# Kernel tuning notes

Hardware: AMD Instinct MI355X
Metric: run time of the kernel (lower is better)

## Reference

```python
import jax, jax.numpy as jnp
import numpy as np

N, D, H, C, E, ED, HID = 50000, 160, 5, 32, 800000, 16, 512
EPS = 1e-5  # torch LayerNorm default
NEG_SLOPE = 0.2  # GATv2Conv default negative_slope


def layer_norm(x, g, b):
    mu = x.mean(-1, keepdims=True)
    var = x.var(-1, keepdims=True)  # biased, matches torch LayerNorm
    return (x - mu) * jax.lax.rsqrt(var + EPS) * g + b


def setup_inputs() -> dict:
    key = jax.random.key(0)
    ks = jax.random.split(key, 12)
    p = lambda k, shape: jax.random.normal(k, shape, jnp.float32) * 0.05
    z = lambda *s: jnp.zeros(s, jnp.float32)
    o = lambda *s: jnp.ones(s, jnp.float32)
    return {
        "x": jax.random.normal(ks[0], (N, D), jnp.float32),
        "edge_index": jax.random.randint(ks[1], (2, E), 0, N),
        "edge_attr": jax.random.normal(ks[2], (E, ED), jnp.float32),
        "u": jax.random.normal(ks[3], (1024, 64), jnp.float32),
        "batch": jax.random.randint(ks[4], (N,), 0, 1024),
        # GATv2Conv params (lin_l, lin_r, lin_edge, att, bias)
        "Wl": p(ks[5], (D, H * C)), "bl": z(H * C),
        "Wr": p(ks[6], (D, H * C)), "br": z(H * C),
        "We": p(ks[7], (ED, H * C)),
        "att": p(ks[8], (H, C)),
        "b_gat": z(H * C),
        # norm1
        "g1": o(D), "b1": z(D),
        # output MLP: Linear(D,HID) -> SELU -> LayerNorm(HID) -> Linear(HID,D)
        "W_m1": p(ks[9], (D, HID)), "b_m1": z(HID),
        "g_m": o(HID), "b_m": z(HID),
        "W_m2": p(ks[10], (HID, D)), "b_m2": z(D),
        # norm2
        "g2": o(D), "b2": z(D),
    }


def reference(x, edge_index, edge_attr, u, batch, Wl, bl, Wr, br, We, att, b_gat,
              g1, b1, W_m1, b_m1, g_m, b_m, W_m2, b_m2, g2, b2):
    src, dst = edge_index[0], edge_index[1]  # messages flow src -> dst
    xl = (x @ Wl + bl).reshape(N, H, C)      # source projection
    xr = (x @ Wr + br).reshape(N, H, C)      # target projection
    ea = (edge_attr @ We).reshape(E, H, C)
    # GATv2 scoring: att . leaky_relu(x_l[j] + x_r[i] + e_ij)
    e = jax.nn.leaky_relu(xl[src] + xr[dst] + ea, NEG_SLOPE)   # [E,H,C]
    score = jnp.einsum('ehc,hc->eh', e, att)                   # [E,H]
    # segment softmax over incoming edges of each target node
    mx = jax.ops.segment_max(score, dst, num_segments=N)       # [N,H]
    ex = jnp.exp(score - mx[dst])
    denom = jax.ops.segment_sum(ex, dst, num_segments=N)
    alpha = ex / denom[dst]                                    # [E,H]
    agg = jax.ops.segment_sum(alpha[:, :, None] * xl[src], dst, num_segments=N)
    attn = agg.reshape(N, H * C) + b_gat                       # concat heads
    # residual + norm, MLP, residual + norm (dropout=0)
    out = layer_norm(x + attn, g1, b1)
    h = layer_norm(jax.nn.selu(out @ W_m1 + b_m1), g_m, b_m)
    mlp = h @ W_m2 + b_m2
    return layer_norm(out + mlp, g2, b2)
```

## Files before the change

### kernel.cpp

```cpp
#include <hip/hip_runtime.h>
#include <math.h>

#define N_NODES 50000
#define D 160
#define H 5
#define C 32
#define HC 160
#define E_EDGES 800000
#define ED 16
#define HID 512
#define EPS 1e-5f
#define NEG_SLOPE 0.2f

typedef __attribute__((ext_vector_type(8))) short bf16x8;
typedef __attribute__((ext_vector_type(4))) float f32x4;
typedef __attribute__((ext_vector_type(4))) short short4v;

__device__ inline float bf2f(short s) {
  unsigned u = ((unsigned)(unsigned short)s) << 16;
  return __builtin_bit_cast(float, u);
}
__device__ inline short f2bf(float f) {
  unsigned u = __builtin_bit_cast(unsigned, f);
  u = u + 0x7fffu + ((u >> 16) & 1u);
  return (short)(u >> 16);
}
__device__ inline float selu_f(float v) {
  return 1.0507009873554805f * (v > 0.f ? v : 1.6732632423543772f * (__expf(v) - 1.f));
}

__global__ void prep_weights(const float* __restrict__ Wl, const float* __restrict__ Wr,
                             const float* __restrict__ Wm1, const float* __restrict__ Wm2,
                             const float* __restrict__ We,
                             short* __restrict__ WlT, short* __restrict__ WrT,
                             short* __restrict__ W1T, short* __restrict__ W2T,
                             short* __restrict__ WeTp) {
  int i = blockIdx.x * blockDim.x + threadIdx.x;
  if (i < 25600) { int n = i / 160, k = i % 160; WlT[n*160 + k] = f2bf(Wl[k*160 + n]); return; }
  i -= 25600;
  if (i < 25600) { int n = i / 160, k = i % 160; WrT[n*160 + k] = f2bf(Wr[k*160 + n]); return; }
  i -= 25600;
  if (i < 81920) { int n = i / 160, k = i % 160; W1T[n*160 + k] = f2bf(Wm1[k*512 + n]); return; }
  i -= 81920;
  if (i < 81920) { int n = i / 512, k = i % 512; W2T[n*512 + k] = f2bf(Wm2[k*160 + n]); return; }
  i -= 81920;
  if (i < 5120) { int col = i / 32, k = i % 32;
    WeTp[col*32 + k] = (k < ED) ? f2bf(We[k*160 + col]) : (short)0; }
}

__global__ void convert_x(const float* __restrict__ x, short* __restrict__ xb) {
  int i = blockIdx.x * blockDim.x + threadIdx.x;
  if (i < N_NODES * D / 8) {
    const float4* s = (const float4*)(x + (size_t)i * 8);
    float4 a = s[0], b = s[1];
    bf16x8 o;
    o[0] = f2bf(a.x); o[1] = f2bf(a.y); o[2] = f2bf(a.z); o[3] = f2bf(a.w);
    o[4] = f2bf(b.x); o[5] = f2bf(b.y); o[6] = f2bf(b.z); o[7] = f2bf(b.w);
    *(bf16x8*)(xb + (size_t)i * 8) = o;
  }
}

__global__ __launch_bounds__(256) void proj_mfma(
    const short* __restrict__ xb, const short* __restrict__ WlT, const short* __restrict__ WrT,
    const float* __restrict__ bl, const float* __restrict__ br,
    short* __restrict__ xl, short* __restrict__ xr)
{
  __shared__ short As[64][40];
  int t = threadIdx.x;
  int wave = t >> 6, lane = t & 63;
  int lq = lane >> 4, lc = lane & 15;
  int row0 = blockIdx.x * 64;
  f32x4 accl[10] = {}, accr[10] = {};
  for (int kt = 0; kt < 5; ++kt) {
    int k0 = kt * 32;
    {
      int r = t >> 2, seg = t & 3;
      int gr = min(row0 + r, N_NODES - 1);
      bf16x8 v = *(const bf16x8*)&xb[(size_t)gr * 160 + k0 + seg * 8];
      *(bf16x8*)&As[r][seg * 8] = v;
    }
    __syncthreads();
    bf16x8 af = *(bf16x8*)&As[wave * 16 + lc][lq * 8];
#pragma unroll
    for (int ct = 0; ct < 10; ++ct) {
      int cc = ct * 16 + lc;
      bf16x8 bfl = *(const bf16x8*)&WlT[cc * 160 + k0 + lq * 8];
      accl[ct] = __builtin_amdgcn_mfma_f32_16x16x32_bf16(af, bfl, accl[ct], 0, 0, 0);
      bf16x8 bfr = *(const bf16x8*)&WrT[cc * 160 + k0 + lq * 8];
      accr[ct] = __builtin_amdgcn_mfma_f32_16x16x32_bf16(af, bfr, accr[ct], 0, 0, 0);
    }
    __syncthreads();
  }
#pragma unroll
  for (int ct = 0; ct < 10; ++ct) {
    int col = ct * 16 + lc;
    float bbl = bl[col], bbr = br[col];
#pragma unroll
    for (int rg = 0; rg < 4; ++rg) {
      int row = row0 + wave * 16 + lq * 4 + rg;
      if (row < N_NODES) {
        xl[(size_t)row * 160 + col] = f2bf(accl[ct][rg] + bbl);
        xr[(size_t)row * 160 + col] = f2bf(accr[ct][rg] + bbr);
      }
    }
  }
}

__global__ void count_kernel(const int* __restrict__ ei, int* __restrict__ cnt) {
  int e = blockIdx.x * blockDim.x + threadIdx.x;
  if (e < E_EDGES) atomicAdd(&cnt[ei[E_EDGES + e]], 1);
}

__global__ __launch_bounds__(1024) void scan_kernel(const int* __restrict__ cnt,
                                                    int* __restrict__ offs) {
  const int PER = (N_NODES + 1023) / 1024;
  int t = threadIdx.x;
  int start = t * PER;
  int sum = 0;
  for (int i = 0; i < PER; ++i) {
    int idx = start + i;
    if (idx < N_NODES) sum += cnt[idx];
  }
  int lane = t & 63, wid = t >> 6;
  int v = sum;
  for (int off = 1; off < 64; off <<= 1) {
    int u = __shfl_up(v, off, 64);
    if (lane >= off) v += u;
  }
  __shared__ int wsums[16];
  if (lane == 63) wsums[wid] = v;
  __syncthreads();
  if (wid == 0) {
    int w = (lane < 16) ? wsums[lane] : 0;
    for (int off = 1; off < 16; off <<= 1) {
      int u = __shfl_up(w, off, 64);
      if (lane >= off) w += u;
    }
    if (lane < 16) wsums[lane] = w;
  }
  __syncthreads();
  int excl = v - sum + (wid > 0 ? wsums[wid - 1] : 0);
  int run = excl;
  for (int i = 0; i < PER; ++i) {
    int idx = start + i;
    if (idx < N_NODES) { offs[idx] = run; run += cnt[idx]; }
  }
  if (t == 1023) offs[N_NODES] = run;
}

__global__ void scatter3(const int* __restrict__ ei, const float* __restrict__ eattr,
                         const int* __restrict__ offs, int* __restrict__ cursor,
                         int* __restrict__ srcm, int* __restrict__ dstm,
                         short* __restrict__ eacsr) {
  int e = blockIdx.x * blockDim.x + threadIdx.x;
  if (e < E_EDGES) {
    int dst = ei[E_EDGES + e];
    int src = ei[e];
    int slot = atomicAdd(&cursor[dst], 1);
    int j = offs[dst] + slot;
    srcm[j] = src * 160;
    dstm[j] = dst * 160;
    const float4* s = (const float4*)&eattr[(size_t)e * ED];
    float4 v0 = s[0], v1 = s[1], v2 = s[2], v3 = s[3];
    short* o = eacsr + (size_t)j * ED;
    short4v w0, w1, w2, w3;
    w0[0]=f2bf(v0.x); w0[1]=f2bf(v0.y); w0[2]=f2bf(v0.z); w0[3]=f2bf(v0.w);
    w1[0]=f2bf(v1.x); w1[1]=f2bf(v1.y); w1[2]=f2bf(v1.z); w1[3]=f2bf(v1.w);
    w2[0]=f2bf(v2.x); w2[1]=f2bf(v2.y); w2[2]=f2bf(v2.z); w2[3]=f2bf(v2.w);
    w3[0]=f2bf(v3.x); w3[1]=f2bf(v3.y); w3[2]=f2bf(v3.z); w3[3]=f2bf(v3.w);
    *(short4v*)(o + 0) = w0; *(short4v*)(o + 4) = w1;
    *(short4v*)(o + 8) = w2; *(short4v*)(o + 12) = w3;
  }
}

__global__ __launch_bounds__(256) void score_mfma(
    const short* __restrict__ eacsr, const int* __restrict__ srcm, const int* __restrict__ dstm,
    const short* __restrict__ WeTp, const short* __restrict__ xl, const short* __restrict__ xr,
    const float* __restrict__ att, float* __restrict__ exj)
{
  int t = threadIdx.x;
  int wave = t >> 6, lane = t & 63;
  int lq = lane >> 4, lc = lane & 15;
  int ebase = blockIdx.x * 64 + wave * 16;
  bf16x8 af = {};
  if (lq < 2) af = *(const bf16x8*)&eacsr[(size_t)(ebase + lc) * ED + lq * 8];
  f32x4 acc[10] = {};
#pragma unroll
  for (int ct = 0; ct < 10; ++ct) {
    bf16x8 bfv = *(const bf16x8*)&WeTp[(ct * 16 + lc) * 32 + lq * 8];
    acc[ct] = __builtin_amdgcn_mfma_f32_16x16x32_bf16(af, bfv, acc[ct], 0, 0, 0);
  }
  int srcv[4], dstv[4];
#pragma unroll
  for (int rg = 0; rg < 4; ++rg) {
    int e = ebase + lq * 4 + rg;
    srcv[rg] = srcm[e];
    dstv[rg] = dstm[e];
  }
  float partial[5][4] = {};
#pragma unroll
  for (int ct = 0; ct < 10; ++ct) {
    int col = ct * 16 + lc;
    float attv = att[col];
#pragma unroll
    for (int rg = 0; rg < 4; ++rg) {
      float z = acc[ct][rg] + bf2f(xl[srcv[rg] + col]) + bf2f(xr[dstv[rg] + col]);
      z = fmaxf(z, NEG_SLOPE * z);
      partial[ct >> 1][rg] = fmaf(z, attv, partial[ct >> 1][rg]);
    }
  }
#pragma unroll
  for (int hh = 0; hh < 5; ++hh) {
#pragma unroll
    for (int rg = 0; rg < 4; ++rg) {
      float p = partial[hh][rg];
      p += __shfl_xor(p, 1, 64);
      p += __shfl_xor(p, 2, 64);
      p += __shfl_xor(p, 4, 64);
      p += __shfl_xor(p, 8, 64);
      if (lc == hh)
        exj[(size_t)hh * E_EDGES + (ebase + lq * 4 + rg)] = __expf(p);
    }
  }
}

__global__ __launch_bounds__(160) void attn_agg(
    const int* __restrict__ srcm, const float* __restrict__ exj,
    const short* __restrict__ xl, const float* __restrict__ x,
    const float* __restrict__ b_gat, const float* __restrict__ g1, const float* __restrict__ b1,
    const int* __restrict__ offs,
    float* __restrict__ outb, short* __restrict__ outb_bf)
{
  int i = blockIdx.x;
  int t = threadIdx.x;
  int e0 = offs[i], e1 = offs[i + 1];
  const float* exph = exj + (size_t)(t >> 5) * E_EDGES;
  float agg = 0.f, denom = 0.f;
  for (int j = e0; j < e1; ++j) {
    float ex = exph[j];
    int sb = srcm[j];
    agg = fmaf(ex, bf2f(xl[sb + t]), agg);
    denom += ex;
  }
  float attn = (denom > 0.f) ? agg / denom : 0.f;
  float val = x[(size_t)i * HC + t] + attn + b_gat[t];
  float s1 = val, s2 = val * val;
#pragma unroll
  for (int m = 16; m >= 1; m >>= 1) { s1 += __shfl_xor(s1, m, 32); s2 += __shfl_xor(s2, m, 32); }
  __shared__ float gs1[5], gs2[5];
  __shared__ float smu, srstd;
  if ((t & 31) == 0) { gs1[t >> 5] = s1; gs2[t >> 5] = s2; }
  __syncthreads();
  if (t == 0) {
    float a = 0.f, b = 0.f;
    for (int g = 0; g < 5; ++g) { a += gs1[g]; b += gs2[g]; }
    float mu = a / 160.f, var = b / 160.f - mu * mu;
    smu = mu; srstd = rsqrtf(var + EPS);
  }
  __syncthreads();
  float o = (val - smu) * srstd * g1[t] + b1[t];
  outb[(size_t)i * HC + t] = o;
  outb_bf[(size_t)i * HC + t] = f2bf(o);
}

__global__ __launch_bounds__(256) void mlp1_mfma(
    const short* __restrict__ ab, const short* __restrict__ W1T,
    const float* __restrict__ b1m, const float* __restrict__ gm, const float* __restrict__ bm,
    short* __restrict__ h)
{
  __shared__ short As[32][40];
  __shared__ float ps1[4][32], ps2[4][32];
  int t = threadIdx.x;
  int wave = t >> 6, lane = t & 63;
  int lq = lane >> 4, lc = lane & 15;
  int row0 = blockIdx.x * 32;
  f32x4 acc[2][8] = {};
  for (int kt = 0; kt < 5; ++kt) {
    int k0 = kt * 32;
    if (t < 128) {
      int r = t >> 2, seg = t & 3;
      int gr = min(row0 + r, N_NODES - 1);
      bf16x8 v = *(const bf16x8*)&ab[(size_t)gr * 160 + k0 + seg * 8];
      *(bf16x8*)&As[r][seg * 8] = v;
    }
    __syncthreads();
    bf16x8 af0 = *(bf16x8*)&As[lc][lq * 8];
    bf16x8 af1 = *(bf16x8*)&As[16 + lc][lq * 8];
#pragma unroll
    for (int ct = 0; ct < 8; ++ct) {
      int cc = wave * 128 + ct * 16 + lc;
      bf16x8 bfv = *(const bf16x8*)&W1T[cc * 160 + k0 + lq * 8];
      acc[0][ct] = __builtin_amdgcn_mfma_f32_16x16x32_bf16(af0, bfv, acc[0][ct], 0, 0, 0);
      acc[1][ct] = __builtin_amdgcn_mfma_f32_16x16x32_bf16(af1, bfv, acc[1][ct], 0, 0, 0);
    }
    __syncthreads();
  }
  float s1[2][4] = {}, s2[2][4] = {};
#pragma unroll
  for (int rt = 0; rt < 2; ++rt)
#pragma unroll
    for (int ct = 0; ct < 8; ++ct)
#pragma unroll
      for (int rg = 0; rg < 4; ++rg) {
        int cc = wave * 128 + ct * 16 + lc;
        float v = selu_f(acc[rt][ct][rg] + b1m[cc]);
        acc[rt][ct][rg] = v;
        s1[rt][rg] += v; s2[rt][rg] += v * v;
      }
#pragma unroll
  for (int m = 1; m <= 8; m <<= 1) {
#pragma unroll
    for (int rt = 0; rt < 2; ++rt)
#pragma unroll
      for (int rg = 0; rg < 4; ++rg) {
        s1[rt][rg] += __shfl_xor(s1[rt][rg], m, 64);
        s2[rt][rg] += __shfl_xor(s2[rt][rg], m, 64);
      }
  }
  if (lc == 0) {
#pragma unroll
    for (int rt = 0; rt < 2; ++rt)
#pragma unroll
      for (int rg = 0; rg < 4; ++rg) {
        ps1[wave][rt * 16 + lq * 4 + rg] = s1[rt][rg];
        ps2[wave][rt * 16 + lq * 4 + rg] = s2[rt][rg];
      }
  }
  __syncthreads();
  float mu[2][4], rstd[2][4];
#pragma unroll
  for (int rt = 0; rt < 2; ++rt)
#pragma unroll
    for (int rg = 0; rg < 4; ++rg) {
      int rl = rt * 16 + lq * 4 + rg;
      float a = ps1[0][rl] + ps1[1][rl] + ps1[2][rl] + ps1[3][rl];
      float b = ps2[0][rl] + ps2[1][rl] + ps2[2][rl] + ps2[3][rl];
      float m_ = a * (1.f / 512.f);
      float var = b * (1.f / 512.f) - m_ * m_;
      mu[rt][rg] = m_; rstd[rt][rg] = rsqrtf(var + EPS);
    }
#pragma unroll
  for (int rt = 0; rt < 2; ++rt)
#pragma unroll
    for (int ct = 0; ct < 8; ++ct)
#pragma unroll
      for (int rg = 0; rg < 4; ++rg) {
        int row = row0 + rt * 16 + lq * 4 + rg;
        int cc = wave * 128 + ct * 16 + lc;
        if (row < N_NODES)
          h[(size_t)row * 512 + cc] =
              f2bf((acc[rt][ct][rg] - mu[rt][rg]) * rstd[rt][rg] * gm[cc] + bm[cc]);
      }
}

__global__ __launch_bounds__(256) void mlp2_mfma(
    const short* __restrict__ hb, const short* __restrict__ W2T,
    const float* __restrict__ b2m, const float* __restrict__ outb,
    const float* __restrict__ g2, const float* __restrict__ b2,
    float* __restrict__ y)
{
  __shared__ short As[64][40];
  int t = threadIdx.x;
  int wave = t >> 6, lane = t & 63;
  int lq = lane >> 4, lc = lane & 15;
  int row0 = blockIdx.x * 64;
  f32x4 acc[10] = {};
  for (int kt = 0; kt < 16; ++kt) {
    int k0 = kt * 32;
    {
      int r = t >> 2, seg = t & 3;
      int gr = min(row0 + r, N_NODES - 1);
      bf16x8 v = *(const bf16x8*)&hb[(size_t)gr * 512 + k0 + seg * 8];
      *(bf16x8*)&As[r][seg * 8] = v;
    }
    __syncthreads();
    bf16x8 af = *(bf16x8*)&As[wave * 16 + lc][lq * 8];
#pragma unroll
    for (int ct = 0; ct < 10; ++ct) {
      int cc = ct * 16 + lc;
      bf16x8 bfv = *(const bf16x8*)&W2T[cc * 512 + k0 + lq * 8];
      acc[ct] = __builtin_amdgcn_mfma_f32_16x16x32_bf16(af, bfv, acc[ct], 0, 0, 0);
    }
    __syncthreads();
  }
  float s1[4] = {}, s2[4] = {};
#pragma unroll
  for (int ct = 0; ct < 10; ++ct) {
    int col = ct * 16 + lc;
#pragma unroll
    for (int rg = 0; rg < 4; ++rg) {
      int rowl = min(row0 + wave * 16 + lq * 4 + rg, N_NODES - 1);
      float v = acc[ct][rg] + b2m[col] + outb[(size_t)rowl * 160 + col];
      acc[ct][rg] = v;
      s1[rg] += v; s2[rg] += v * v;
    }
  }
#pragma unroll
  for (int m = 1; m <= 8; m <<= 1) {
#pragma unroll
    for (int rg = 0; rg < 4; ++rg) {
      s1[rg] += __shfl_xor(s1[rg], m, 64);
      s2[rg] += __shfl_xor(s2[rg], m, 64);
    }
  }
  float mu[4], rstd[4];
#pragma unroll
  for (int rg = 0; rg < 4; ++rg) {
    float m_ = s1[rg] * (1.f / 160.f);
    float var = s2[rg] * (1.f / 160.f) - m_ * m_;
    mu[rg] = m_; rstd[rg] = rsqrtf(var + EPS);
  }
#pragma unroll
  for (int ct = 0; ct < 10; ++ct) {
    int col = ct * 16 + lc;
#pragma unroll
    for (int rg = 0; rg < 4; ++rg) {
      int row = row0 + wave * 16 + lq * 4 + rg;
      if (row < N_NODES)
        y[(size_t)row * 160 + col] = (acc[ct][rg] - mu[rg]) * rstd[rg] * g2[col] + b2[col];
    }
  }
}

extern "C" void kernel_launch(void* const* d_in, const int* in_sizes, int n_in,
                              void* d_out, int out_size, void* d_ws, size_t ws_size,
                              hipStream_t stream) {
  const float* x     = (const float*)d_in[0];
  const int*   ei    = (const int*)d_in[1];
  const float* eattr = (const float*)d_in[2];
  const float* Wl    = (const float*)d_in[5];
  const float* bl    = (const float*)d_in[6];
  const float* Wr    = (const float*)d_in[7];
  const float* br    = (const float*)d_in[8];
  const float* We    = (const float*)d_in[9];
  const float* att   = (const float*)d_in[10];
  const float* bgat  = (const float*)d_in[11];
  const float* g1    = (const float*)d_in[12];
  const float* b1    = (const float*)d_in[13];
  const float* Wm1   = (const float*)d_in[14];
  const float* bm1   = (const float*)d_in[15];
  const float* gm    = (const float*)d_in[16];
  const float* bm    = (const float*)d_in[17];
  const float* Wm2   = (const float*)d_in[18];
  const float* bm2   = (const float*)d_in[19];
  const float* g2    = (const float*)d_in[20];
  const float* b2    = (const float*)d_in[21];
  float* y = (float*)d_out;

  char* p = (char*)d_ws;
  auto alloc = [&](size_t bytes) {
    void* q = p;
    p += (bytes + 255) & ~(size_t)255;
    return q;
  };
  short* xb      = (short*)alloc((size_t)N_NODES * 160 * 2);
  short* xlb     = (short*)alloc((size_t)N_NODES * 160 * 2);
  short* xrb     = (short*)alloc((size_t)N_NODES * 160 * 2);
  float* outb    = (float*)alloc((size_t)N_NODES * 160 * 4);
  short* outb_bf = (short*)alloc((size_t)N_NODES * 160 * 2);
  short* hb      = (short*)alloc((size_t)N_NODES * 512 * 2);
  short* eacsr   = (short*)alloc((size_t)E_EDGES * ED * 2);
  int*   srcm    = (int*)alloc((size_t)E_EDGES * 4);
  int*   dstm    = (int*)alloc((size_t)E_EDGES * 4);
  float* exj     = (float*)alloc((size_t)H * E_EDGES * 4);
  short* WlT     = (short*)alloc(160 * 160 * 2);
  short* WrT     = (short*)alloc(160 * 160 * 2);
  short* W1T     = (short*)alloc(512 * 160 * 2);
  short* W2T     = (short*)alloc(160 * 512 * 2);
  short* WeTp    = (short*)alloc(160 * 32 * 2);
  int*   cnt     = (int*)alloc((size_t)N_NODES * 4);
  int*   offs    = (int*)alloc((size_t)(N_NODES + 1) * 4);
  int*   cursor  = (int*)alloc((size_t)N_NODES * 4);

  hipMemsetAsync(cnt, 0, (size_t)N_NODES * 4, stream);
  hipMemsetAsync(cursor, 0, (size_t)N_NODES * 4, stream);

  prep_weights<<<(220160 + 255) / 256, 256, 0, stream>>>(Wl, Wr, Wm1, Wm2, We,
                                                         WlT, WrT, W1T, W2T, WeTp);
  convert_x<<<(N_NODES * 160 / 8 + 255) / 256, 256, 0, stream>>>(x, xb);
  count_kernel<<<(E_EDGES + 255) / 256, 256, 0, stream>>>(ei, cnt);
  scan_kernel<<<1, 1024, 0, stream>>>(cnt, offs);
  scatter3<<<(E_EDGES + 255) / 256, 256, 0, stream>>>(ei, eattr, offs, cursor,
                                                      srcm, dstm, eacsr);
  proj_mfma<<<(N_NODES + 63) / 64, 256, 0, stream>>>(xb, WlT, WrT, bl, br, xlb, xrb);
  score_mfma<<<E_EDGES / 64, 256, 0, stream>>>(eacsr, srcm, dstm, WeTp, xlb, xrb, att, exj);
  attn_agg<<<N_NODES, 160, 0, stream>>>(srcm, exj, xlb, x, bgat, g1, b1, offs, outb, outb_bf);
  mlp1_mfma<<<(N_NODES + 31) / 32, 256, 0, stream>>>(outb_bf, W1T, bm1, gm, bm, hb);
  mlp2_mfma<<<(N_NODES + 63) / 64, 256, 0, stream>>>(hb, W2T, bm2, outb, g2, b2, y);
}
```

Baseline: 811.8 us.

## Fuse edge scoring with softmax aggregation per node; retile mlp2 to 128 rows

Merges the per-edge score kernel and the per-node aggregation kernel into one wave-per-node kernel. It computes edge scores with MFMA over chunks of 16 incoming edges, accumulates exp-weighted xl and the denominators in registers, then applies LayerNorm. This removes the exj buffer and the dstm array, along with their global writes and reads and the second gather of xl rows. The cost is load imbalance from varying node degree and wasted lanes on low-degree nodes. Separately, mlp2 now processes 128 rows per block with a 64-wide K step, so each W2T fragment is reused across two row tiles.

```diff
diff --git a/kernel.cpp b/kernel.cpp
--- a/kernel.cpp
+++ b/kernel.cpp
@@ -150,8 +150,7 @@
 
 __global__ void scatter3(const int* __restrict__ ei, const float* __restrict__ eattr,
                          const int* __restrict__ offs, int* __restrict__ cursor,
-                         int* __restrict__ srcm, int* __restrict__ dstm,
-                         short* __restrict__ eacsr) {
+                         int* __restrict__ srcm, short* __restrict__ eacsr) {
   int e = blockIdx.x * blockDim.x + threadIdx.x;
   if (e < E_EDGES) {
     int dst = ei[E_EDGES + e];
@@ -159,7 +158,6 @@
     int slot = atomicAdd(&cursor[dst], 1);
     int j = offs[dst] + slot;
     srcm[j] = src * 160;
-    dstm[j] = dst * 160;
     const float4* s = (const float4*)&eattr[(size_t)e * ED];
     float4 v0 = s[0], v1 = s[1], v2 = s[2], v3 = s[3];
     short* o = eacsr + (size_t)j * ED;
@@ -173,94 +171,116 @@
   }
 }
 
-__global__ __launch_bounds__(256) void score_mfma(
-    const short* __restrict__ eacsr, const int* __restrict__ srcm, const int* __restrict__ dstm,
+__global__ __launch_bounds__(256) void attn_fused(
+    const short* __restrict__ eacsr, const int* __restrict__ srcm,
     const short* __restrict__ WeTp, const short* __restrict__ xl, const short* __restrict__ xr,
-    const float* __restrict__ att, float* __restrict__ exj)
+    const float* __restrict__ att, const float* __restrict__ x,
+    const float* __restrict__ b_gat, const float* __restrict__ g1, const float* __restrict__ b1,
+    const int* __restrict__ offs,
+    float* __restrict__ outb, short* __restrict__ outb_bf)
 {
   int t = threadIdx.x;
   int wave = t >> 6, lane = t & 63;
   int lq = lane >> 4, lc = lane & 15;
-  int ebase = blockIdx.x * 64 + wave * 16;
-  bf16x8 af = {};
-  if (lq < 2) af = *(const bf16x8*)&eacsr[(size_t)(ebase + lc) * ED + lq * 8];
-  f32x4 acc[10] = {};
+  int i = blockIdx.x * 4 + wave;
+  int e0 = offs[i], e1 = offs[i + 1];
+
+  float xrv[10], attv[10];
 #pragma unroll
   for (int ct = 0; ct < 10; ++ct) {
-    bf16x8 bfv = *(const bf16x8*)&WeTp[(ct * 16 + lc) * 32 + lq * 8];
-    acc[ct] = __builtin_amdgcn_mfma_f32_16x16x32_bf16(af, bfv, acc[ct], 0, 0, 0);
-  }
-  int srcv[4], dstv[4];
-#pragma unroll
-  for (int rg = 0; rg < 4; ++rg) {
-    int e = ebase + lq * 4 + rg;
-    srcv[rg] = srcm[e];
-    dstv[rg] = dstm[e];
-  }
-  float partial[5][4] = {};
+    xrv[ct] = bf2f(xr[(size_t)i * 160 + ct * 16 + lc]);
+    attv[ct] = att[ct * 16 + lc];
+  }
+  float aggc[10] = {};
+  float den[5] = {};
+  const f32x4 zero4 = {};
+
+  for (int j0 = e0; j0 < e1; j0 += 16) {
+    bf16x8 af = {};
+    if (lq < 2) {
+      int jr = min(j0 + lc, e1 - 1);
+      af = *(const bf16x8*)&eacsr[(size_t)jr * ED + lq * 8];
+    }
+    f32x4 acc[10];
+#pragma unroll
+    for (int ct = 0; ct < 10; ++ct) {
+      bf16x8 bfv = *(const bf16x8*)&WeTp[(ct * 16 + lc) * 32 + lq * 8];
+      acc[ct] = __builtin_amdgcn_mfma_f32_16x16x32_bf16(af, bfv, zero4, 0, 0, 0);
+    }
+    int src[4]; bool ok[4];
+#pragma unroll
+    for (int rg = 0; rg < 4; ++rg) {
+      int j = j0 + lq * 4 + rg;
+      ok[rg] = (j < e1);
+      src[rg] = srcm[min(j, e1 - 1)];
+    }
+    float xlv[10][4];
+    float partial[5][4] = {};
+#pragma unroll
+    for (int ct = 0; ct < 10; ++ct) {
+#pragma unroll
+      for (int rg = 0; rg < 4; ++rg) {
+        float v = bf2f(xl[src[rg] + ct * 16 + lc]);
+        xlv[ct][rg] = v;
+        float z = acc[ct][rg] + v + xrv[ct];
+        z = fmaxf(z, NEG_SLOPE * z);
+        partial[ct >> 1][rg] = fmaf(z, attv[ct], partial[ct >> 1][rg]);
+      }
+    }
+#pragma unroll
+    for (int hh = 0; hh < 5; ++hh) {
+#pragma unroll
+      for (int rg = 0; rg < 4; ++rg) {
+        float p = partial[hh][rg];
+        p += __shfl_xor(p, 1, 64);
+        p += __shfl_xor(p, 2, 64);
+        p += __shfl_xor(p, 4, 64);
+        p += __shfl_xor(p, 8, 64);
+        float ex = ok[rg] ? __expf(p) : 0.f;
+        den[hh] += ex;
+        partial[hh][rg] = ex;
+      }
+    }
+#pragma unroll
+    for (int ct = 0; ct < 10; ++ct)
+#pragma unroll
+      for (int rg = 0; rg < 4; ++rg)
+        aggc[ct] = fmaf(partial[ct >> 1][rg], xlv[ct][rg], aggc[ct]);
+  }
 #pragma unroll
   for (int ct = 0; ct < 10; ++ct) {
-    int col = ct * 16 + lc;
-    float attv = att[col];
-#pragma unroll
-    for (int rg = 0; rg < 4; ++rg) {
-      float z = acc[ct][rg] + bf2f(xl[srcv[rg] + col]) + bf2f(xr[dstv[rg] + col]);
-      z = fmaxf(z, NEG_SLOPE * z);
-      partial[ct >> 1][rg] = fmaf(z, attv, partial[ct >> 1][rg]);
-    }
+    aggc[ct] += __shfl_xor(aggc[ct], 16, 64);
+    aggc[ct] += __shfl_xor(aggc[ct], 32, 64);
   }
 #pragma unroll
   for (int hh = 0; hh < 5; ++hh) {
-#pragma unroll
-    for (int rg = 0; rg < 4; ++rg) {
-      float p = partial[hh][rg];
-      p += __shfl_xor(p, 1, 64);
-      p += __shfl_xor(p, 2, 64);
-      p += __shfl_xor(p, 4, 64);
-      p += __shfl_xor(p, 8, 64);
-      if (lc == hh)
-        exj[(size_t)hh * E_EDGES + (ebase + lq * 4 + rg)] = __expf(p);
-    }
-  }
-}
-
-__global__ __launch_bounds__(160) void attn_agg(
-    const int* __restrict__ srcm, const float* __restrict__ exj,
-    const short* __restrict__ xl, const float* __restrict__ x,
-    const float* __restrict__ b_gat, const float* __restrict__ g1, const float* __restrict__ b1,
-    const int* __restrict__ offs,
-    float* __restrict__ outb, short* __restrict__ outb_bf)
-{
-  int i = blockIdx.x;
-  int t = threadIdx.x;
-  int e0 = offs[i], e1 = offs[i + 1];
-  const float* exph = exj + (size_t)(t >> 5) * E_EDGES;
-  float agg = 0.f, denom = 0.f;
-  for (int j = e0; j < e1; ++j) {
-    float ex = exph[j];
-    int sb = srcm[j];
-    agg = fmaf(ex, bf2f(xl[sb + t]), agg);
-    denom += ex;
-  }
-  float attn = (denom > 0.f) ? agg / denom : 0.f;
-  float val = x[(size_t)i * HC + t] + attn + b_gat[t];
-  float s1 = val, s2 = val * val;
-#pragma unroll
-  for (int m = 16; m >= 1; m >>= 1) { s1 += __shfl_xor(s1, m, 32); s2 += __shfl_xor(s2, m, 32); }
-  __shared__ float gs1[5], gs2[5];
-  __shared__ float smu, srstd;
-  if ((t & 31) == 0) { gs1[t >> 5] = s1; gs2[t >> 5] = s2; }
-  __syncthreads();
-  if (t == 0) {
-    float a = 0.f, b = 0.f;
-    for (int g = 0; g < 5; ++g) { a += gs1[g]; b += gs2[g]; }
-    float mu = a / 160.f, var = b / 160.f - mu * mu;
-    smu = mu; srstd = rsqrtf(var + EPS);
-  }
-  __syncthreads();
-  float o = (val - smu) * srstd * g1[t] + b1[t];
-  outb[(size_t)i * HC + t] = o;
-  outb_bf[(size_t)i * HC + t] = f2bf(o);
+    den[hh] += __shfl_xor(den[hh], 16, 64);
+    den[hh] += __shfl_xor(den[hh], 32, 64);
+  }
+  float val[10];
+  float s1 = 0.f, s2 = 0.f;
+#pragma unroll
+  for (int ct = 0; ct < 10; ++ct) {
+    float d = den[ct >> 1];
+    float attn = (d > 0.f) ? aggc[ct] / d : 0.f;
+    float v = x[(size_t)i * 160 + ct * 16 + lc] + attn + b_gat[ct * 16 + lc];
+    val[ct] = v;
+    s1 += v; s2 += v * v;
+  }
+#pragma unroll
+  for (int m = 1; m <= 8; m <<= 1) { s1 += __shfl_xor(s1, m, 64); s2 += __shfl_xor(s2, m, 64); }
+  float mu = s1 * (1.f / 160.f);
+  float var = s2 * (1.f / 160.f) - mu * mu;
+  float rstd = rsqrtf(var + EPS);
+  if (lq == 0) {
+#pragma unroll
+    for (int ct = 0; ct < 10; ++ct) {
+      int col = ct * 16 + lc;
+      float o = (val[ct] - mu) * rstd * g1[col] + b1[col];
+      outb[(size_t)i * 160 + col] = o;
+      outb_bf[(size_t)i * 160 + col] = f2bf(o);
+    }
+  }
 }
 
 __global__ __launch_bounds__(256) void mlp1_mfma(
@@ -359,67 +379,80 @@
     const float* __restrict__ g2, const float* __restrict__ b2,
     float* __restrict__ y)
 {
-  __shared__ short As[64][40];
+  __shared__ short As[128][72];
   int t = threadIdx.x;
   int wave = t >> 6, lane = t & 63;
   int lq = lane >> 4, lc = lane & 15;
-  int row0 = blockIdx.x * 64;
-  f32x4 acc[10] = {};
-  for (int kt = 0; kt < 16; ++kt) {
-    int k0 = kt * 32;
-    {
-      int r = t >> 2, seg = t & 3;
+  int row0 = blockIdx.x * 128;
+  f32x4 acc[2][10] = {};
+  for (int kt = 0; kt < 8; ++kt) {
+    int k0 = kt * 64;
+    __syncthreads();
+#pragma unroll
+    for (int q = 0; q < 4; ++q) {
+      int idx = t + 256 * q;
+      int r = idx >> 3, seg = idx & 7;
       int gr = min(row0 + r, N_NODES - 1);
-      bf16x8 v = *(const bf16x8*)&hb[(size_t)gr * 512 + k0 + seg * 8];
-      *(bf16x8*)&As[r][seg * 8] = v;
+      *(bf16x8*)&As[r][seg * 8] = *(const bf16x8*)&hb[(size_t)gr * 512 + k0 + seg * 8];
     }
     __syncthreads();
-    bf16x8 af = *(bf16x8*)&As[wave * 16 + lc][lq * 8];
+#pragma unroll
+    for (int ks = 0; ks < 2; ++ks) {
+      bf16x8 af0 = *(bf16x8*)&As[wave * 32 + lc][ks * 32 + lq * 8];
+      bf16x8 af1 = *(bf16x8*)&As[wave * 32 + 16 + lc][ks * 32 + lq * 8];
+#pragma unroll
+      for (int ct = 0; ct < 10; ++ct) {
+        bf16x8 bfv = *(const bf16x8*)&W2T[(ct * 16 + lc) * 512 + k0 + ks * 32 + lq * 8];
+        acc[0][ct] = __builtin_amdgcn_mfma_f32_16x16x32_bf16(af0, bfv, acc[0][ct], 0, 0, 0);
+        acc[1][ct] = __builtin_amdgcn_mfma_f32_16x16x32_bf16(af1, bfv, acc[1][ct], 0, 0, 0);
+      }
+    }
+  }
+  float s1[2][4] = {}, s2[2][4] = {};
+#pragma unroll
+  for (int rt = 0; rt < 2; ++rt)
 #pragma unroll
     for (int ct = 0; ct < 10; ++ct) {
-      int cc = ct * 16 + lc;
-      bf16x8 bfv = *(const bf16x8*)&W2T[cc * 512 + k0 + lq * 8];
-      acc[ct] = __builtin_amdgcn_mfma_f32_16x16x32_bf16(af, bfv, acc[ct], 0, 0, 0);
-    }
-    __syncthreads();
-  }
-  float s1[4] = {}, s2[4] = {};
-#pragma unroll
-  for (int ct = 0; ct < 10; ++ct) {
-    int col = ct * 16 + lc;
+      int col = ct * 16 + lc;
+#pragma unroll
+      for (int rg = 0; rg < 4; ++rg) {
+        int rowl = min(row0 + wave * 32 + rt * 16 + lq * 4 + rg, N_NODES - 1);
+        float v = acc[rt][ct][rg] + b2m[col] + outb[(size_t)rowl * 160 + col];
+        acc[rt][ct][rg] = v;
+        s1[rt][rg] += v; s2[rt][rg] += v * v;
+      }
+    }
+#pragma unroll
+  for (int m = 1; m <= 8; m <<= 1) {
+#pragma unroll
+    for (int rt = 0; rt < 2; ++rt)
+#pragma unroll
+      for (int rg = 0; rg < 4; ++rg) {
+        s1[rt][rg] += __shfl_xor(s1[rt][rg], m, 64);
+        s2[rt][rg] += __shfl_xor(s2[rt][rg], m, 64);
+      }
+  }
+  float mu[2][4], rstd[2][4];
+#pragma unroll
+  for (int rt = 0; rt < 2; ++rt)
 #pragma unroll
     for (int rg = 0; rg < 4; ++rg) {
-      int rowl = min(row0 + wave * 16 + lq * 4 + rg, N_NODES - 1);
-      float v = acc[ct][rg] + b2m[col] + outb[(size_t)rowl * 160 + col];
-      acc[ct][rg] = v;
-      s1[rg] += v; s2[rg] += v * v;
-    }
-  }
-#pragma unroll
-  for (int m = 1; m <= 8; m <<= 1) {
-#pragma unroll
-    for (int rg = 0; rg < 4; ++rg) {
-      s1[rg] += __shfl_xor(s1[rg], m, 64);
-      s2[rg] += __shfl_xor(s2[rg], m, 64);
-    }
-  }
-  float mu[4], rstd[4];
-#pragma unroll
-  for (int rg = 0; rg < 4; ++rg) {
-    float m_ = s1[rg] * (1.f / 160.f);
-    float var = s2[rg] * (1.f / 160.f) - m_ * m_;
-    mu[rg] = m_; rstd[rg] = rsqrtf(var + EPS);
-  }
-#pragma unroll
-  for (int ct = 0; ct < 10; ++ct) {
-    int col = ct * 16 + lc;
-#pragma unroll
-    for (int rg = 0; rg < 4; ++rg) {
-      int row = row0 + wave * 16 + lq * 4 + rg;
-      if (row < N_NODES)
-        y[(size_t)row * 160 + col] = (acc[ct][rg] - mu[rg]) * rstd[rg] * g2[col] + b2[col];
-    }
-  }
+      float m_ = s1[rt][rg] * (1.f / 160.f);
+      float var = s2[rt][rg] * (1.f / 160.f) - m_ * m_;
+      mu[rt][rg] = m_; rstd[rt][rg] = rsqrtf(var + EPS);
+    }
+#pragma unroll
+  for (int rt = 0; rt < 2; ++rt)
+#pragma unroll
+    for (int ct = 0; ct < 10; ++ct) {
+      int col = ct * 16 + lc;
+#pragma unroll
+      for (int rg = 0; rg < 4; ++rg) {
+        int row = row0 + wave * 32 + rt * 16 + lq * 4 + rg;
+        if (row < N_NODES)
+          y[(size_t)row * 160 + col] = (acc[rt][ct][rg] - mu[rt][rg]) * rstd[rt][rg] * g2[col] + b2[col];
+      }
+    }
 }
 
 extern "C" void kernel_launch(void* const* d_in, const int* in_sizes, int n_in,
@@ -461,8 +494,6 @@
   short* hb      = (short*)alloc((size_t)N_NODES * 512 * 2);
   short* eacsr   = (short*)alloc((size_t)E_EDGES * ED * 2);
   int*   srcm    = (int*)alloc((size_t)E_EDGES * 4);
-  int*   dstm    = (int*)alloc((size_t)E_EDGES * 4);
-  float* exj     = (float*)alloc((size_t)H * E_EDGES * 4);
   short* WlT     = (short*)alloc(160 * 160 * 2);
   short* WrT     = (short*)alloc(160 * 160 * 2);
   short* W1T     = (short*)alloc(512 * 160 * 2);
@@ -480,11 +511,10 @@
   convert_x<<<(N_NODES * 160 / 8 + 255) / 256, 256, 0, stream>>>(x, xb);
   count_kernel<<<(E_EDGES + 255) / 256, 256, 0, stream>>>(ei, cnt);
   scan_kernel<<<1, 1024, 0, stream>>>(cnt, offs);
-  scatter3<<<(E_EDGES + 255) / 256, 256, 0, stream>>>(ei, eattr, offs, cursor,
-                                                      srcm, dstm, eacsr);
+  scatter3<<<(E_EDGES + 255) / 256, 256, 0, stream>>>(ei, eattr, offs, cursor, srcm, eacsr);
   proj_mfma<<<(N_NODES + 63) / 64, 256, 0, stream>>>(xb, WlT, WrT, bl, br, xlb, xrb);
-  score_mfma<<<E_EDGES / 64, 256, 0, stream>>>(eacsr, srcm, dstm, WeTp, xlb, xrb, att, exj);
-  attn_agg<<<N_NODES, 160, 0, stream>>>(srcm, exj, xlb, x, bgat, g1, b1, offs, outb, outb_bf);
+  attn_fused<<<N_NODES / 4, 256, 0, stream>>>(eacsr, srcm, WeTp, xlb, xrb, att, x,
+                                              bgat, g1, b1, offs, outb, outb_bf);
   mlp1_mfma<<<(N_NODES + 31) / 32, 256, 0, stream>>>(outb_bf, W1T, bm1, gm, bm, hb);
-  mlp2_mfma<<<(N_NODES + 63) / 64, 256, 0, stream>>>(hb, W2T, bm2, outb, g2, b2, y);
-}
+  mlp2_mfma<<<(N_NODES + 127) / 128, 256, 0, stream>>>(hb, W2T, bm2, outb, g2, b2, y);
+}
```

New measurement: 783.3 us. 3.5% less time.
